# Optimization experiments

Hardware: AMD Instinct MI355X
Metric: run time of the kernel (lower is better)

Reference implementation:

```python
import jax, jax.numpy as jnp
import numpy as np

BETA = 5.0
NEG = jnp.float32(-1e30)  # finite stand-in for -inf; avoids NaN on the fully-masked row 0


def setup_inputs() -> dict:
    key = jax.random.key(0)
    ks = jax.random.split(key, 6)
    B, L, d, dv, dh = 4, 4096, 512, 512, 512
    K = jax.random.normal(ks[0], (B, L, d), dtype=jnp.float32)
    V = jax.random.normal(ks[1], (B, L, dv), dtype=jnp.float32)
    # nn.Linear weights: shape (out, in), applied as x @ W.T
    Wq = jax.random.normal(ks[2], (dh, d), dtype=jnp.float32) / np.sqrt(d).astype(np.float32)
    Wk = jax.random.normal(ks[3], (dh, d), dtype=jnp.float32) / np.sqrt(d).astype(np.float32)
    Wv = jax.random.normal(ks[4], (dv, dv), dtype=jnp.float32) / np.sqrt(dv).astype(np.float32)
    Wo = jax.random.normal(ks[5], (dv, dv), dtype=jnp.float32) / np.sqrt(dv).astype(np.float32)
    return {"K": K, "V": V, "Wq": Wq, "Wk": Wk, "Wv": Wv, "Wo": Wo}


def reference(K, V, Wq, Wk, Wv, Wo):
    B, L, _ = K.shape
    dh = Wq.shape[0]
    Qh = jnp.einsum('bld,hd->blh', K, Wq)
    Kh = jnp.einsum('bld,hd->blh', K, Wk)
    Vp = jnp.einsum('bld,ed->ble', V, Wv)
    scale = jnp.float32(BETA) / jnp.sqrt(jnp.float32(dh))
    scores = jnp.einsum('bih,bjh->bij', Qh, Kh) * scale  # [B,L,L]
    # strict causal mask: attend only to j <= i-1 (triu with diagonal=0 masked)
    mask = jnp.triu(jnp.ones((L, L), dtype=bool), k=0)
    scores = jnp.where(mask[None], NEG, scores)
    attn = jax.nn.softmax(scores, axis=-1)
    # row 0 has no past: torch code zeroes it after softmax
    attn = attn.at[:, 0, :].set(0.0)
    out = jnp.einsum('bij,bjd->bid', attn, Vp)
    Vhat = jnp.einsum('bld,ed->ble', out, Wo)
    return Vhat
```

## Files before the change

kernel.cpp:

```cpp
#include <hip/hip_runtime.h>


typedef unsigned short u16;
typedef _Float16 f16;
typedef short short8 __attribute__((ext_vector_type(8)));
typedef _Float16 half8 __attribute__((ext_vector_type(8)));
typedef _Float16 half4 __attribute__((ext_vector_type(4)));
typedef float floatx4 __attribute__((ext_vector_type(4)));

#define L_SEQ 4096
#define NBATCH 4
#define DMODEL 512
#define SCALE 0.22097086912079612f
#define MMAX 30.0f

__device__ __forceinline__ u16 f2bf(float f) {
  unsigned int u = __float_as_uint(f);
  u += 0x7fffu + ((u >> 16) & 1u);
  return (u16)(u >> 16);
}
__device__ __forceinline__ float bf2f(u16 h) {
  return __uint_as_float(((unsigned int)h) << 16);
}

__device__ __forceinline__ void gl2lds16(const void* g, void* l) {
  __builtin_amdgcn_global_load_lds(
      (const __attribute__((address_space(1))) unsigned int*)g,
      (__attribute__((address_space(3))) unsigned int*)l, 16, 0, 0);
}

__global__ __launch_bounds__(256) void cvt_f16_x2(
    const float4* __restrict__ x0, half4* __restrict__ o0,
    const float4* __restrict__ x1, half4* __restrict__ o1, int n4) {
  int i = blockIdx.x * 256 + threadIdx.x;
  if (i >= n4) return;
  const float4* __restrict__ x = blockIdx.y ? x1 : x0;
  half4* __restrict__ o = blockIdx.y ? o1 : o0;
  float4 f = x[i];
  half4 h = {(f16)f.x, (f16)f.y, (f16)f.z, (f16)f.w};
  o[i] = h;
}

__global__ __launch_bounds__(256) void cvt_f16_x4(
    const float4* __restrict__ x0, half4* __restrict__ o0,
    const float4* __restrict__ x1, half4* __restrict__ o1,
    const float4* __restrict__ x2, half4* __restrict__ o2,
    const float4* __restrict__ x3, half4* __restrict__ o3, int n4) {
  int i = blockIdx.x * 256 + threadIdx.x;
  if (i >= n4) return;
  const float4* __restrict__ x = (blockIdx.y & 2) ? ((blockIdx.y & 1) ? x3 : x2)
                                                  : ((blockIdx.y & 1) ? x1 : x0);
  half4* __restrict__ o = (blockIdx.y & 2) ? ((blockIdx.y & 1) ? o3 : o2)
                                           : ((blockIdx.y & 1) ? o1 : o0);
  float4 f = x[i];
  half4 h = {(f16)f.x, (f16)f.y, (f16)f.z, (f16)f.w};
  o[i] = h;
}

template <int OUT_MODE>
__global__ __launch_bounds__(256, 2) void gemm128(
    const f16* __restrict__ A, const f16* __restrict__ B,
    void* __restrict__ Cout, int ldc, long sAz, long sBz, long sCz) {
  __shared__ f16 sA[2][128 * 64];
  __shared__ f16 sB[2][128 * 64];

  const int tid = threadIdx.x;
  const int wave = tid >> 6, lane = tid & 63, quad = lane >> 4, l16 = lane & 15;
  const int wm = (wave >> 1) * 64, wn = (wave & 1) * 64;
  const int bn = blockIdx.x * 128, bm = blockIdx.y * 128, bz = blockIdx.z;

  const f16* Ab = A + (long)bz * sAz + (long)bm * 512;
  const f16* Bb = B + (long)bz * sBz + (long)bn * 512;

  floatx4 zero = {0.f, 0.f, 0.f, 0.f};
  floatx4 acc[4][4];
#pragma unroll
  for (int mi = 0; mi < 4; mi++)
#pragma unroll
    for (int ni = 0; ni < 4; ni++) acc[mi][ni] = zero;

  const int lrow = lane >> 3;
  auto stage = [&](int bs, int ks) {
#pragma unroll
    for (int i = 0; i < 4; i++) {
      int r0 = wave * 32 + i * 8;
      int r = r0 + lrow;
      int c = ((lane & 7) - r) & 7;
      gl2lds16(Ab + (long)r * 512 + ks * 64 + c * 8, &sA[bs][r0 * 64]);
      gl2lds16(Bb + (long)r * 512 + ks * 64 + c * 8, &sB[bs][r0 * 64]);
    }
  };

  stage(0, 0);
  for (int ks = 0; ks < 8; ks++) {
    const int cur = ks & 1;
    __syncthreads();
    if (ks + 1 < 8) stage(cur ^ 1, ks + 1);

#pragma unroll
    for (int kk = 0; kk < 2; kk++) {
      half8 af[4], bf[4];
#pragma unroll
      for (int mi = 0; mi < 4; mi++) {
        int row = wm + mi * 16 + l16;
        int slot = (kk * 4 + quad + row) & 7;
        af[mi] = *(const half8*)&sA[cur][row * 64 + slot * 8];
      }
#pragma unroll
      for (int ni = 0; ni < 4; ni++) {
        int row = wn + ni * 16 + l16;
        int slot = (kk * 4 + quad + row) & 7;
        bf[ni] = *(const half8*)&sB[cur][row * 64 + slot * 8];
      }
#pragma unroll
      for (int mi = 0; mi < 4; mi++)
#pragma unroll
        for (int ni = 0; ni < 4; ni++)
          acc[mi][ni] = __builtin_amdgcn_mfma_f32_16x16x32_f16(
              af[mi], bf[ni], acc[mi][ni], 0, 0, 0);
    }
  }

#pragma unroll
  for (int mi = 0; mi < 4; mi++) {
#pragma unroll
    for (int ni = 0; ni < 4; ni++) {
#pragma unroll
      for (int rr = 0; rr < 4; rr++) {
        int row = bm + wm + mi * 16 + quad * 4 + rr;
        int col = bn + wn + ni * 16 + l16;
        long idx = (long)bz * sCz + (long)row * ldc + col;
        float v = acc[mi][ni][rr];
        if (OUT_MODE == 1) {
          ((f16*)Cout)[idx] = (f16)v;
        } else if (OUT_MODE == 3) {
          ((u16*)Cout)[idx] = f2bf(v);
        } else {
          ((float*)Cout)[idx] = v;
        }
      }
    }
  }
}

__device__ __forceinline__ int nseg_of(int qt) {
  return (qt < 12) ? ((qt + 2) >> 1) : ((qt + 4) >> 2);
}
__device__ __forceinline__ int seg_off(int qt) {
  int o = 0;
  for (int q = 2; q < qt; q++) o += 4 * nseg_of(q);
  return o;
}

#define SV_LD 40

__global__ __launch_bounds__(512, 2) void attn_kernel(
    const f16* __restrict__ Qh_g, const f16* __restrict__ Kh_g,
    const u16* __restrict__ VpT, f16* __restrict__ Ob,
    u16* __restrict__ Opart, float* __restrict__ ml) {
  __shared__ f16 sK[2][32 * 512];
  __shared__ u16 sV[2][512 * 32];
  __shared__ u16 sP[8 * 16 * SV_LD];
  __shared__ float sL[128];

  const int tid = threadIdx.x;
  const int wave = tid >> 6, lane = tid & 63, quad = lane >> 4, l16 = lane & 15;

  int id = blockIdx.x;
  int qt = 31;
  for (;;) {
    int c = 4 * nseg_of(qt);
    if (id < c) break;
    id -= c;
    qt--;
  }
  const int S = nseg_of(qt);
  const int b = id / S;
  const int s = id - b * S;
  const int ktn = 4 * qt + 4;
  const int base = ktn / S, rem = ktn - base * S;
  const int len = base + (s < rem);
  const int start = s * base + (s < rem ? s : rem);

  const int q0 = qt * 128 + wave * 16;
  const long qbase = (long)b * L_SEQ + q0;

  half8 qf[16];
#pragma unroll
  for (int c = 0; c < 16; c++) {
    long a = (qbase + l16) * 512 + c * 32 + quad * 8;
    qf[c] = *(const half8*)&Qh_g[a];
  }

  floatx4 zero = {0.f, 0.f, 0.f, 0.f};
  float l_run[4] = {0.f, 0.f, 0.f, 0.f};
  floatx4 oacc[32];
#pragma unroll
  for (int nb = 0; nb < 32; nb++) oacc[nb] = zero;

  const f16* __restrict__ Kh_b = Kh_g + (long)b * L_SEQ * 512;
  const u16* __restrict__ V_b  = VpT + (long)b * (512L * L_SEQ);

  auto stage = [&](int bs, int jt) {
    const int j0 = jt * 32;
#pragma unroll
    for (int i = 0; i < 4; i++) {
      int r = wave * 4 + i;
      int k = (lane - (r & 7)) & 63;
      gl2lds16(Kh_b + (long)(j0 + r) * 512 + k * 8, &sK[bs][r * 512]);
    }
#pragma unroll
    for (int i = 0; i < 4; i++) {
      int g = wave * 4 + i;
      int d = g * 16 + (lane >> 2);
      int c = ((lane & 3) - d) & 3;
      gl2lds16(V_b + (long)d * L_SEQ + j0 + c * 8, &sV[bs][g * 512]);
    }
  };

  stage(0, start);

  for (int v = 0; v < len; v++) {
    const int j0 = (start + v) * 32;
    const int cur = v & 1;

    __syncthreads();
    if (v + 1 < len) stage(cur ^ 1, start + v + 1);

    const f16* kc = &sK[cur][0];
    const u16* vc = &sV[cur][0];

    floatx4 sacc0 = zero, sacc1 = zero;
    const int rot = l16 & 7;
#pragma unroll
    for (int c = 0; c < 16; c++) {
      int slot = (c * 4 + quad + rot) & 63;
      half8 b0 = *(const half8*)&kc[l16 * 512 + slot * 8];
      half8 b1 = *(const half8*)&kc[(16 + l16) * 512 + slot * 8];
      sacc0 = __builtin_amdgcn_mfma_f32_16x16x32_f16(qf[c], b0, sacc0, 0, 0, 0);
      sacc1 = __builtin_amdgcn_mfma_f32_16x16x32_f16(qf[c], b1, sacc1, 0, 0, 0);
    }

#pragma unroll
    for (int rr = 0; rr < 4; rr++) {
      int irow = q0 + quad * 4 + rr;
      float s0 = fmaf(sacc0[rr], SCALE, -MMAX);
      float s1 = fmaf(sacc1[rr], SCALE, -MMAX);
      if (j0 + l16 >= irow) s0 = -1e30f;
      if (j0 + 16 + l16 >= irow) s1 = -1e30f;
      float p0 = __expf(s0);
      float p1 = __expf(s1);
      l_run[rr] += p0 + p1;
      int pb = wave * (16 * SV_LD) + (quad * 4 + rr) * SV_LD;
      sP[pb + l16] = f2bf(p0);
      sP[pb + 16 + l16] = f2bf(p1);
    }

    __builtin_amdgcn_sched_barrier(0);
    __builtin_amdgcn_s_waitcnt(0xC07F);
    __builtin_amdgcn_s_barrier();
    __builtin_amdgcn_sched_barrier(0);

    short8 vf[4];
#pragma unroll
    for (int nbl = 0; nbl < 4; nbl++) {
      int dvr = wave * 64 + nbl * 16 + l16;
      vf[nbl] = *(const short8*)&vc[dvr * 32 + ((quad + l16) & 3) * 8];
    }
#pragma unroll
    for (int qg = 0; qg < 8; qg++) {
      short8 ap = *(const short8*)&sP[qg * (16 * SV_LD) + l16 * SV_LD + quad * 8];
#pragma unroll
      for (int nbl = 0; nbl < 4; nbl++)
        oacc[qg * 4 + nbl] =
            __builtin_amdgcn_mfma_f32_16x16x32_bf16(ap, vf[nbl], oacc[qg * 4 + nbl], 0, 0, 0);
    }
  }

#pragma unroll
  for (int rr = 0; rr < 4; rr++) {
    float l = l_run[rr];
    l += __shfl_xor(l, 1);
    l += __shfl_xor(l, 2);
    l += __shfl_xor(l, 4);
    l += __shfl_xor(l, 8);
    l_run[rr] = l;
  }
  if (l16 == 0) {
#pragma unroll
    for (int rr = 0; rr < 4; rr++) sL[wave * 16 + quad * 4 + rr] = l_run[rr];
  }
  __syncthreads();

  if (S == 1) {
#pragma unroll
    for (int qg = 0; qg < 8; qg++) {
#pragma unroll
      for (int rr = 0; rr < 4; rr++) {
        int row = qg * 16 + quad * 4 + rr;
        int irow = qt * 128 + row;
        float lv = sL[row];
        float inv = (irow == 0 || lv <= 0.f) ? 0.f : 1.0f / lv;
        long obase = ((long)b * L_SEQ + irow) * 512 + wave * 64;
#pragma unroll
        for (int nbl = 0; nbl < 4; nbl++)
          Ob[obase + nbl * 16 + l16] = (f16)(oacc[qg * 4 + nbl][rr] * inv);
      }
    }
  } else {
    const int slot = seg_off(qt) + b * S + s;
    const long obase0 = (long)slot * (128 * 512);
#pragma unroll
    for (int qg = 0; qg < 8; qg++) {
#pragma unroll
      for (int rr = 0; rr < 4; rr++) {
        int row = qg * 16 + quad * 4 + rr;
        long ob = obase0 + (long)row * 512 + wave * 64;
#pragma unroll
        for (int nbl = 0; nbl < 4; nbl++)
          Opart[ob + nbl * 16 + l16] = f2bf(oacc[qg * 4 + nbl][rr]);
      }
    }
    if (l16 == 0) {
#pragma unroll
      for (int rr = 0; rr < 4; rr++)
        ml[slot * 128 + wave * 16 + quad * 4 + rr] = l_run[rr];
    }
  }
}

__global__ __launch_bounds__(256) void attn_combine(
    const u16* __restrict__ Opart, const float* __restrict__ ml,
    f16* __restrict__ Ob) {
  const int qt = 2 + (blockIdx.x >> 2), b = blockIdx.x & 3;
  const int S = nseg_of(qt);
  const int bslot = seg_off(qt) + b * S;
  __shared__ float sInv[128];
  const int tid = threadIdx.x;
  if (tid < 128) {
    int row = tid, irow = qt * 128 + row;
    float ltot = 0.f;
    for (int s = 0; s < S; s++) ltot += ml[(bslot + s) * 128 + row];
    sInv[row] = (irow == 0 || ltot <= 0.f) ? 0.f : 1.0f / ltot;
  }
  __syncthreads();
  const int c0 = blockIdx.y * 16;
  for (int idx = tid; idx < 128 * 16; idx += 256) {
    int row = idx >> 4, cc = c0 + (idx & 15);
    float acc[8] = {0, 0, 0, 0, 0, 0, 0, 0};
    for (int s = 0; s < S; s++) {
      int4 pk = *(const int4*)&Opart[(long)(bslot + s) * 65536 + row * 512 + cc * 8];
      const u16* ph = (const u16*)&pk;
#pragma unroll
      for (int e = 0; e < 8; e++) acc[e] += bf2f(ph[e]);
    }
    float inv = sInv[row];
    f16 o[8];
#pragma unroll
    for (int e = 0; e < 8; e++) o[e] = (f16)(acc[e] * inv);
    *(int4*)&Ob[((long)b * L_SEQ + qt * 128 + row) * 512 + cc * 8] = *(int4*)o;
  }
}

extern "C" void kernel_launch(void* const* d_in, const int* in_sizes, int n_in,
                              void* d_out, int out_size, void* d_ws, size_t ws_size,
                              hipStream_t stream) {
  const float* K  = (const float*)d_in[0];
  const float* V  = (const float*)d_in[1];
  const float* Wq = (const float*)d_in[2];
  const float* Wk = (const float*)d_in[3];
  const float* Wv = (const float*)d_in[4];
  const float* Wo = (const float*)d_in[5];
  float* out = (float*)d_out;

  const int NKV = NBATCH * L_SEQ * DMODEL;
  const int NW = DMODEL * DMODEL;
  const int NSLOT = 640;

  char* w = (char*)d_ws;
  size_t off = 0;
  auto carve = [&](size_t bytes) {
    void* p = w + off;
    off += (bytes + 255) & ~(size_t)255;
    return p;
  };
  f16* Qh   = (f16*)carve((size_t)NKV * 2);
  f16* Kh   = (f16*)carve((size_t)NKV * 2);
  u16* VpTw = (u16*)carve((size_t)NKV * 2);
  f16* Obw  = (f16*)carve((size_t)NKV * 2);
  f16* Wo16 = (f16*)carve((size_t)NW * 2);
  float* mlw = (float*)carve((size_t)NSLOT * 128 * 4);
  u16* Opart = (u16*)carve((size_t)NSLOT * 65536 * 2);
  f16* K16  = (f16*)Opart;
  f16* V16  = K16 + NKV;
  f16* Wq16 = V16 + NKV;
  f16* Wk16 = Wq16 + NW;
  f16* Wv16 = Wk16 + NW;

  cvt_f16_x2<<<dim3(NKV / 1024, 2, 1), 256, 0, stream>>>(
      (const float4*)K, (half4*)K16, (const float4*)V, (half4*)V16, NKV / 4);
  cvt_f16_x4<<<dim3(NW / 1024, 4, 1), 256, 0, stream>>>(
      (const float4*)Wq, (half4*)Wq16, (const float4*)Wk, (half4*)Wk16,
      (const float4*)Wv, (half4*)Wv16, (const float4*)Wo, (half4*)Wo16, NW / 4);

  gemm128<1><<<dim3(4, 128, 2), 256, 0, stream>>>(
      K16, Wq16, (void*)Qh, 512, 0, (long)NW, (long)NKV);

  gemm128<3><<<dim3(32, 4, NBATCH), 256, 0, stream>>>(
      Wv16, V16, (void*)VpTw, L_SEQ, 0, (long)L_SEQ * 512, (long)512 * L_SEQ);

  attn_kernel<<<dim3(648, 1, 1), 512, 0, stream>>>(
      Qh, Kh, VpTw, Obw, Opart, mlw);
  attn_combine<<<dim3(120, 4, 1), 256, 0, stream>>>(Opart, mlw, Obw);

  gemm128<2><<<dim3(4, 128, 1), 256, 0, stream>>>(
      Obw, Wo16, (void*)out, 512, 0, 0, 0);

  (void)in_sizes; (void)n_in; (void)out_size; (void)ws_size;
}
```

Baseline: 350.0 us.

## Fold Wq and Wk into one matrix so attention uses raw K as keys

```diff
diff --git a/kernel.cpp b/kernel.cpp
--- a/kernel.cpp
+++ b/kernel.cpp
@@ -29,32 +29,53 @@
       (__attribute__((address_space(3))) unsigned int*)l, 16, 0, 0);
 }
 
-__global__ __launch_bounds__(256) void cvt_f16_x2(
+__global__ __launch_bounds__(256) void cvt_f16_x4b(
     const float4* __restrict__ x0, half4* __restrict__ o0,
-    const float4* __restrict__ x1, half4* __restrict__ o1, int n4) {
+    const float4* __restrict__ x1, half4* __restrict__ o1, int n4a,
+    const float4* __restrict__ x2, half4* __restrict__ o2,
+    const float4* __restrict__ x3, half4* __restrict__ o3, int n4b) {
   int i = blockIdx.x * 256 + threadIdx.x;
+  int y = blockIdx.y;
+  const float4* __restrict__ x;
+  half4* __restrict__ o;
+  int n4;
+  if (y == 0)      { x = x0; o = o0; n4 = n4a; }
+  else if (y == 1) { x = x1; o = o1; n4 = n4a; }
+  else if (y == 2) { x = x2; o = o2; n4 = n4b; }
+  else             { x = x3; o = o3; n4 = n4b; }
   if (i >= n4) return;
-  const float4* __restrict__ x = blockIdx.y ? x1 : x0;
-  half4* __restrict__ o = blockIdx.y ? o1 : o0;
   float4 f = x[i];
   half4 h = {(f16)f.x, (f16)f.y, (f16)f.z, (f16)f.w};
   o[i] = h;
 }
 
-__global__ __launch_bounds__(256) void cvt_f16_x4(
-    const float4* __restrict__ x0, half4* __restrict__ o0,
-    const float4* __restrict__ x1, half4* __restrict__ o1,
-    const float4* __restrict__ x2, half4* __restrict__ o2,
-    const float4* __restrict__ x3, half4* __restrict__ o3, int n4) {
-  int i = blockIdx.x * 256 + threadIdx.x;
-  if (i >= n4) return;
-  const float4* __restrict__ x = (blockIdx.y & 2) ? ((blockIdx.y & 1) ? x3 : x2)
-                                                  : ((blockIdx.y & 1) ? x1 : x0);
-  half4* __restrict__ o = (blockIdx.y & 2) ? ((blockIdx.y & 1) ? o3 : o2)
-                                           : ((blockIdx.y & 1) ? o1 : o0);
-  float4 f = x[i];
-  half4 h = {(f16)f.x, (f16)f.y, (f16)f.z, (f16)f.w};
-  o[i] = h;
+__global__ __launch_bounds__(256) void cvt_t16(
+    const float* __restrict__ x0, f16* __restrict__ o0,
+    const float* __restrict__ x1, f16* __restrict__ o1) {
+  const float* __restrict__ x = blockIdx.z ? x1 : x0;
+  f16* __restrict__ o = blockIdx.z ? o1 : o0;
+  __shared__ f16 t[64][72];
+  const int r0 = blockIdx.y * 64, c0 = blockIdx.x * 64;
+  const int tr = threadIdx.x >> 4, tc4 = (threadIdx.x & 15) * 4;
+#pragma unroll
+  for (int it = 0; it < 4; it++) {
+    int r = tr + it * 16;
+    float4 v = *(const float4*)&x[(long)(r0 + r) * 512 + c0 + tc4];
+    t[tc4 + 0][r] = (f16)v.x;
+    t[tc4 + 1][r] = (f16)v.y;
+    t[tc4 + 2][r] = (f16)v.z;
+    t[tc4 + 3][r] = (f16)v.w;
+  }
+  __syncthreads();
+  const int wr = threadIdx.x >> 3, wc8 = (threadIdx.x & 7) * 8;
+#pragma unroll
+  for (int it = 0; it < 2; it++) {
+    int rr = wr + it * 32;
+    half8 h;
+#pragma unroll
+    for (int e = 0; e < 8; e++) h[e] = t[rr][wc8 + e];
+    *(half8*)&o[(long)(c0 + rr) * 512 + r0 + wc8] = h;
+  }
 }
 
 template <int OUT_MODE>
@@ -213,7 +234,7 @@
     for (int i = 0; i < 4; i++) {
       int g = wave * 4 + i;
       int d = g * 16 + (lane >> 2);
-      int c = ((lane & 3) - d) & 3;
+      int c = ((lane & 3) - (d + (d >> 2))) & 3;
       gl2lds16(V_b + (long)d * L_SEQ + j0 + c * 8, &sV[bs][g * 512]);
     }
   };
@@ -265,7 +286,7 @@
 #pragma unroll
     for (int nbl = 0; nbl < 4; nbl++) {
       int dvr = wave * 64 + nbl * 16 + l16;
-      vf[nbl] = *(const short8*)&vc[dvr * 32 + ((quad + l16) & 3) * 8];
+      vf[nbl] = *(const short8*)&vc[dvr * 32 + ((quad + l16 + (l16 >> 2)) & 3) * 8];
     }
 #pragma unroll
     for (int qg = 0; qg < 8; qg++) {
@@ -385,32 +406,34 @@
     return p;
   };
   f16* Qh   = (f16*)carve((size_t)NKV * 2);
-  f16* Kh   = (f16*)carve((size_t)NKV * 2);
+  f16* K16  = (f16*)carve((size_t)NKV * 2);
   u16* VpTw = (u16*)carve((size_t)NKV * 2);
   f16* Obw  = (f16*)carve((size_t)NKV * 2);
   f16* Wo16 = (f16*)carve((size_t)NW * 2);
+  f16* MTw  = (f16*)carve((size_t)NW * 2);
   float* mlw = (float*)carve((size_t)NSLOT * 128 * 4);
   u16* Opart = (u16*)carve((size_t)NSLOT * 65536 * 2);
-  f16* K16  = (f16*)Opart;
-  f16* V16  = K16 + NKV;
-  f16* Wq16 = V16 + NKV;
-  f16* Wk16 = Wq16 + NW;
-  f16* Wv16 = Wk16 + NW;
-
-  cvt_f16_x2<<<dim3(NKV / 1024, 2, 1), 256, 0, stream>>>(
-      (const float4*)K, (half4*)K16, (const float4*)V, (half4*)V16, NKV / 4);
-  cvt_f16_x4<<<dim3(NW / 1024, 4, 1), 256, 0, stream>>>(
-      (const float4*)Wq, (half4*)Wq16, (const float4*)Wk, (half4*)Wk16,
+  f16* V16   = (f16*)Opart;
+  f16* WqT16 = V16 + NKV;
+  f16* WkT16 = WqT16 + NW;
+  f16* Wv16  = WkT16 + NW;
+
+  cvt_f16_x4b<<<dim3(NKV / 1024, 4, 1), 256, 0, stream>>>(
+      (const float4*)K, (half4*)K16, (const float4*)V, (half4*)V16, NKV / 4,
       (const float4*)Wv, (half4*)Wv16, (const float4*)Wo, (half4*)Wo16, NW / 4);
-
-  gemm128<1><<<dim3(4, 128, 2), 256, 0, stream>>>(
-      K16, Wq16, (void*)Qh, 512, 0, (long)NW, (long)NKV);
+  cvt_t16<<<dim3(8, 8, 2), 256, 0, stream>>>(Wq, WqT16, Wk, WkT16);
+
+  gemm128<1><<<dim3(4, 4, 1), 256, 0, stream>>>(
+      WkT16, WqT16, (void*)MTw, 512, 0, 0, 0);
+
+  gemm128<1><<<dim3(4, 128, 1), 256, 0, stream>>>(
+      K16, MTw, (void*)Qh, 512, 0, 0, 0);
 
   gemm128<3><<<dim3(32, 4, NBATCH), 256, 0, stream>>>(
       Wv16, V16, (void*)VpTw, L_SEQ, 0, (long)L_SEQ * 512, (long)512 * L_SEQ);
 
   attn_kernel<<<dim3(648, 1, 1), 512, 0, stream>>>(
-      Qh, Kh, VpTw, Obw, Opart, mlw);
+      Qh, K16, VpTw, Obw, Opart, mlw);
   attn_combine<<<dim3(120, 4, 1), 256, 0, stream>>>(Opart, mlw, Obw);
 
   gemm128<2><<<dim3(4, 128, 1), 256, 0, stream>>>(
```

After: 350.2 us. About the same (+0.1%).
